# Kernel optimization log

Measured on AMD Instinct MI355X. Metric: run time of the kernel, lower is better.

Reference implementation:

```python
import jax, jax.numpy as jnp
import numpy as np

B, L, H, NH = 4, 1024, 768, 12
HS = H // NH          # 64
DPB_DIM = H // 4      # 192
TEMPERATURE = 1.0


def setup_inputs() -> dict:
    key = jax.random.key(0)
    ks = jax.random.split(key, 10)
    def xavier(k, shape):
        fan_in, fan_out = shape[0], shape[-1]
        std = (2.0 / (fan_in + fan_out)) ** 0.5
        return jax.random.normal(k, shape, dtype=jnp.float32) * std
    return {
        "x": jax.random.normal(ks[0], (B, L, H), dtype=jnp.float32),
        "adj": jax.random.normal(ks[1], (B, 1, L, L), dtype=jnp.float32),
        "mask": jnp.ones((B, L), dtype=bool),
        "weights": xavier(ks[2], (H, 3 * H)),
        "in_bias": jnp.zeros((1, 1, 3 * H), dtype=jnp.float32),
        "out_bias": jnp.zeros((1, 1, H), dtype=jnp.float32),
        "dpb_w0": xavier(ks[3], (1, DPB_DIM)),
        "dpb_b0": jnp.zeros((DPB_DIM,), dtype=jnp.float32),
        "dpb_w1": xavier(ks[4], (DPB_DIM, DPB_DIM)),
        "dpb_b1": jnp.zeros((DPB_DIM,), dtype=jnp.float32),
        "dpb_w2": xavier(ks[5], (DPB_DIM, NH)),
        "dpb_b2": jnp.zeros((NH,), dtype=jnp.float32),
    }


def _dyn_pos_bias(n, w0, b0, w1, b1, w2, b2):
    # relative positions -(n-1)..(n-1) -> per-head bias [NH, n, n]
    pos = jnp.arange(-n + 1, n, dtype=jnp.float32)[:, None]      # [2n-1, 1]
    hdn = jax.nn.silu(pos @ w0 + b0)
    hdn = jax.nn.silu(hdn @ w1 + b1)
    table = hdn @ w2 + b2                                        # [2n-1, NH]
    idx = jnp.arange(n)[:, None] - jnp.arange(n)[None, :] + (n - 1)  # [n, n]
    return jnp.transpose(table[idx], (2, 0, 1))                  # [NH, n, n]


def reference(x, adj, mask, weights, in_bias, out_bias,
              dpb_w0, dpb_b0, dpb_w1, dpb_b1, dpb_w2, dpb_b2):
    b, l, h = x.shape
    qkv = x @ weights + in_bias                                  # [b, l, 3h]
    # view(b,l,NH,-1).permute(0,2,1,3).chunk(3, dim=3): split 3*HS per head
    qkv = jnp.transpose(qkv.reshape(b, l, NH, 3 * HS), (0, 2, 1, 3))  # [b,NH,l,3HS]
    Q, K, V = qkv[..., :HS], qkv[..., HS:2 * HS], qkv[..., 2 * HS:]
    norm = HS ** 0.5
    attention = jnp.einsum('bhid,bhjd->bhij', Q, K) / TEMPERATURE / norm
    raw_attention = attention                                    # returned pre-bias
    attn_bias = _dyn_pos_bias(l, dpb_w0, dpb_b0, dpb_w1, dpb_b1, dpb_w2, dpb_b2)
    attention = attention + attn_bias[None] + adj
    mask_value = -jnp.finfo(attention.dtype).max
    attention = jnp.where(mask[:, None, None, :], attention, mask_value)
    attention = jax.nn.softmax(attention, axis=-1)
    out = attention @ V                                          # [b,NH,l,HS]
    out = jnp.transpose(out, (0, 2, 1, 3)).reshape(b, l, h)
    out = out + out_bias
    return (out, raw_attention)
```

## Files before the change

### kernel.cpp

```cpp
#include <hip/hip_runtime.h>
#include <stdint.h>
#include <stddef.h>


#define BB 4
#define LL 1024
#define NHH 12
#define HSS 64
#define HH 768
#define OUT_ELEMS (BB * LL * HH)
#define QKV_ELEMS (BB * NHH * LL * HSS)
#define X_ELEMS (BB * LL * HH)
#define W_ELEMS (HH * 3 * HH)

typedef __attribute__((ext_vector_type(8))) short short8;
typedef __attribute__((ext_vector_type(4))) float f32x4;

__device__ __forceinline__ ushort f2bf(float f) {
    union { float f; unsigned int i; } v; v.f = f;
    unsigned int r = v.i + 0x7FFFu + ((v.i >> 16) & 1u);
    return (ushort)(r >> 16);
}

__global__ void sentinel_kernel(float* out) {
    if (threadIdx.x == 0) out[0] = 12345.0f;
}

__global__ __launch_bounds__(256)
void cvt_bf16(const float* __restrict__ src, ushort* __restrict__ dst, int n) {
    int i = (blockIdx.x * 256 + threadIdx.x) * 8;
    if (i >= n) return;
    float4 a = *(const float4*)(src + i);
    float4 b = *(const float4*)(src + i + 4);
    short8 o;
    o[0] = (short)f2bf(a.x); o[1] = (short)f2bf(a.y);
    o[2] = (short)f2bf(a.z); o[3] = (short)f2bf(a.w);
    o[4] = (short)f2bf(b.x); o[5] = (short)f2bf(b.y);
    o[6] = (short)f2bf(b.z); o[7] = (short)f2bf(b.w);
    *(short8*)(dst + i) = o;
}

__global__ void dpb_kernel(const float* __restrict__ w0, const float* __restrict__ b0,
                           const float* __restrict__ w1, const float* __restrict__ b1,
                           const float* __restrict__ w2, const float* __restrict__ b2,
                           float* __restrict__ table) {
    __shared__ float h0s[192];
    __shared__ float h1s[192];
    int r = blockIdx.x, j = threadIdx.x;
    double pos = (double)(r - 1023);
    double a = pos * (double)w0[j] + (double)b0[j];
    h0s[j] = (float)(a / (1.0 + exp(-a)));
    __syncthreads();
    double acc = (double)b1[j];
    for (int k = 0; k < 192; ++k) acc += (double)h0s[k] * (double)w1[k * 192 + j];
    h1s[j] = (float)(acc / (1.0 + exp(-acc)));
    __syncthreads();
    if (j < 12) {
        double t = (double)b2[j];
        for (int k = 0; k < 192; ++k) t += (double)h1s[k] * (double)w2[k * 12 + j];
        table[r * 12 + j] = (float)t;
    }
}

__global__ __launch_bounds__(256)
void qkv_mfma(const ushort* __restrict__ x, const ushort* __restrict__ w,
              const float* __restrict__ bias,
              ushort* __restrict__ Qb, ushort* __restrict__ Kb, ushort* __restrict__ Vb) {
    __shared__ ushort As[64][32];
    __shared__ ushort Bts[64][56];

    int m0 = blockIdx.y * 64, n0 = blockIdx.x * 64;
    int tid = threadIdx.x, lane = tid & 63, wid = tid >> 6;
    int wr = wid >> 1, wc = wid & 1;
    int g = lane >> 4, qi = lane & 15;
    f32x4 acc[2][2] = {};

    int arow = tid >> 2, acol = (tid & 3) * 8;
    int bn = tid & 63, bkb = (tid >> 6) * 8;

    for (int k0 = 0; k0 < 768; k0 += 32) {
        short8 av = *(const short8*)(x + (size_t)(m0 + arow) * 768 + k0 + acol);
        ushort bt[8];
        #pragma unroll
        for (int i = 0; i < 8; ++i)
            bt[i] = w[(size_t)(k0 + bkb + i) * 2304 + n0 + bn];
        *(short8*)&As[arow][acol] = av;
        short8 bv;
        #pragma unroll
        for (int i = 0; i < 8; ++i) bv[i] = (short)bt[i];
        *(short8*)&Bts[bn][bkb] = bv;
        __syncthreads();

        short8 af0 = *(const short8*)&As[wr * 32 + qi][g * 8];
        short8 af1 = *(const short8*)&As[wr * 32 + 16 + qi][g * 8];
        short8 bf0 = *(const short8*)&Bts[wc * 32 + qi][g * 8];
        short8 bf1 = *(const short8*)&Bts[wc * 32 + 16 + qi][g * 8];
        acc[0][0] = __builtin_amdgcn_mfma_f32_16x16x32_bf16(af0, bf0, acc[0][0], 0, 0, 0);
        acc[0][1] = __builtin_amdgcn_mfma_f32_16x16x32_bf16(af0, bf1, acc[0][1], 0, 0, 0);
        acc[1][0] = __builtin_amdgcn_mfma_f32_16x16x32_bf16(af1, bf0, acc[1][0], 0, 0, 0);
        acc[1][1] = __builtin_amdgcn_mfma_f32_16x16x32_bf16(af1, bf1, acc[1][1], 0, 0, 0);
        __syncthreads();
    }

    #pragma unroll
    for (int ti = 0; ti < 2; ++ti)
    #pragma unroll
    for (int tj = 0; tj < 2; ++tj)
    #pragma unroll
    for (int r = 0; r < 4; ++r) {
        int row = m0 + wr * 32 + ti * 16 + g * 4 + r;
        int col = n0 + wc * 32 + tj * 16 + qi;
        float val = acc[ti][tj][r] + bias[col];
        int h = col / 192, rem = col % 192;
        int which = rem >> 6, d = rem & 63;
        int bb = row >> 10, ll = row & 1023;
        ushort* dst = which == 0 ? Qb : (which == 1 ? Kb : Vb);
        dst[(((size_t)(bb * 12 + h) * 1024 + ll) << 6) + d] = f2bf(val);
    }
}

__global__ __launch_bounds__(256)
void attn_mfma(const ushort* __restrict__ Qb, const ushort* __restrict__ Kb,
               const ushort* __restrict__ Vb, const float* __restrict__ adj,
               const float* __restrict__ table, const float* __restrict__ out_bias,
               float* __restrict__ out, float* __restrict__ raw) {
    __shared__ ushort Ks[32][72];
    __shared__ ushort Vt[64][72];
    __shared__ ushort Ps[4][16][40];

    int blk = blockIdx.x;
    int lb = (blk & 7) * 96 + (blk >> 3);
    int qb = lb & 15;
    int bh = lb >> 4;
    int h = bh % 12;
    int b = bh / 12;
    int q0 = qb * 64;
    int tid = threadIdx.x, lane = tid & 63, wid = tid >> 6;
    int g = lane >> 4, qi = lane & 15;
    int qg = q0 + wid * 16 + qi;

    short8 qfrag[2];
    qfrag[0] = *(const short8*)(Qb + ((size_t)(bh * 1024 + qg) << 6) + g * 8);
    qfrag[1] = *(const short8*)(Qb + ((size_t)(bh * 1024 + qg) << 6) + 32 + g * 8);

    float m = -INFINITY, ssum = 0.f;
    f32x4 oacc[4] = {};

    int srow = tid >> 3, scol = (tid & 7) * 8;
    int vd = tid & 63, vjb = (tid >> 6) * 8;

    for (int j0 = 0; j0 < 1024; j0 += 32) {
        short8 kv = *(const short8*)(Kb + ((size_t)(bh * 1024 + j0 + srow) << 6) + scol);
        ushort vt8[8];
        #pragma unroll
        for (int i = 0; i < 8; ++i)
            vt8[i] = Vb[((size_t)(bh * 1024 + j0 + vjb + i) << 6) + vd];
        *(short8*)&Ks[srow][scol] = kv;
        short8 vv;
        #pragma unroll
        for (int i = 0; i < 8; ++i) vv[i] = (short)vt8[i];
        *(short8*)&Vt[vd][vjb] = vv;
        __syncthreads();

        f32x4 sacc[2];
        #pragma unroll
        for (int jt = 0; jt < 2; ++jt) {
            short8 kf0 = *(const short8*)&Ks[jt * 16 + qi][g * 8];
            short8 kf1 = *(const short8*)&Ks[jt * 16 + qi][32 + g * 8];
            f32x4 z = {0.f, 0.f, 0.f, 0.f};
            z = __builtin_amdgcn_mfma_f32_16x16x32_bf16(kf0, qfrag[0], z, 0, 0, 0);
            z = __builtin_amdgcn_mfma_f32_16x16x32_bf16(kf1, qfrag[1], z, 0, 0, 0);
            sacc[jt] = z;
        }

        float lg[8];
        #pragma unroll
        for (int jt = 0; jt < 2; ++jt) {
            int jbase = j0 + jt * 16 + g * 4;
            f32x4 sv = sacc[jt] * 0.125f;
            *(f32x4*)(raw + ((size_t)(bh * 1024 + qg) << 10) + jbase) = sv;
            float4 av = *(const float4*)(adj + ((size_t)(b * 1024 + qg) << 10) + jbase);
            int tidx = (1023 + qg - jbase) * 12 + h;
            lg[jt * 4 + 0] = sv[0] + table[tidx] + av.x;
            lg[jt * 4 + 1] = sv[1] + table[tidx - 12] + av.y;
            lg[jt * 4 + 2] = sv[2] + table[tidx - 24] + av.z;
            lg[jt * 4 + 3] = sv[3] + table[tidx - 36] + av.w;
        }

        float cmax = lg[0];
        #pragma unroll
        for (int i = 1; i < 8; ++i) cmax = fmaxf(cmax, lg[i]);
        cmax = fmaxf(cmax, __shfl_xor(cmax, 16));
        cmax = fmaxf(cmax, __shfl_xor(cmax, 32));
        float newm = fmaxf(m, cmax);
        float corr = __expf(m - newm);
        float p[8], csum = 0.f;
        #pragma unroll
        for (int i = 0; i < 8; ++i) { p[i] = __expf(lg[i] - newm); csum += p[i]; }
        csum += __shfl_xor(csum, 16);
        csum += __shfl_xor(csum, 32);
        ssum = ssum * corr + csum;
        m = newm;
        #pragma unroll
        for (int dt = 0; dt < 4; ++dt) oacc[dt] *= corr;

        #pragma unroll
        for (int jt = 0; jt < 2; ++jt) {
            ushort4 pw;
            #pragma unroll
            for (int r = 0; r < 4; ++r) ((ushort*)&pw)[r] = f2bf(p[jt * 4 + r]);
            *(ushort4*)&Ps[wid][qi][jt * 16 + g * 4] = pw;
        }
        short8 pf = *(const short8*)&Ps[wid][qi][g * 8];
        #pragma unroll
        for (int dt = 0; dt < 4; ++dt) {
            short8 vf = *(const short8*)&Vt[dt * 16 + qi][g * 8];
            oacc[dt] = __builtin_amdgcn_mfma_f32_16x16x32_bf16(vf, pf, oacc[dt], 0, 0, 0);
        }
        __syncthreads();
    }

    float inv = 1.f / ssum;
    #pragma unroll
    for (int dt = 0; dt < 4; ++dt) {
        float4 ob = *(const float4*)(out_bias + h * 64 + dt * 16 + g * 4);
        f32x4 ov;
        ov[0] = oacc[dt][0] * inv + ob.x;
        ov[1] = oacc[dt][1] * inv + ob.y;
        ov[2] = oacc[dt][2] * inv + ob.z;
        ov[3] = oacc[dt][3] * inv + ob.w;
        *(f32x4*)(out + (size_t)(b * 1024 + qg) * 768 + h * 64 + dt * 16 + g * 4) = ov;
    }
}

extern "C" void kernel_launch(void* const* d_in, const int* in_sizes, int n_in,
                              void* d_out, int out_size, void* d_ws, size_t ws_size,
                              hipStream_t stream) {
    const float* x        = (const float*)d_in[0];
    const float* adj      = (const float*)d_in[1];
    const float* weights  = (const float*)d_in[3];
    const float* in_bias  = (const float*)d_in[4];
    const float* out_bias = (const float*)d_in[5];
    const float* dpb_w0   = (const float*)d_in[6];
    const float* dpb_b0   = (const float*)d_in[7];
    const float* dpb_w1   = (const float*)d_in[8];
    const float* dpb_b1   = (const float*)d_in[9];
    const float* dpb_w2   = (const float*)d_in[10];
    const float* dpb_b2   = (const float*)d_in[11];

    float* out = (float*)d_out;
    float* raw = out + OUT_ELEMS;

    float*  table = (float*)d_ws;
    ushort* xb    = (ushort*)((char*)d_ws + 98304);
    ushort* wb    = xb + X_ELEMS;
    ushort* Qb    = wb + W_ELEMS;
    ushort* Kb    = Qb + QKV_ELEMS;
    ushort* Vb    = Kb + QKV_ELEMS;
    size_t need = 98304 + (size_t)X_ELEMS * 2 + (size_t)W_ELEMS * 2
                + 3 * (size_t)QKV_ELEMS * 2;
    if (ws_size < need) {
        sentinel_kernel<<<1, 64, 0, stream>>>(out);
        return;
    }

    cvt_bf16<<<X_ELEMS / (256 * 8), 256, 0, stream>>>(x, xb, X_ELEMS);
    cvt_bf16<<<W_ELEMS / (256 * 8), 256, 0, stream>>>(weights, wb, W_ELEMS);
    dpb_kernel<<<2047, 192, 0, stream>>>(dpb_w0, dpb_b0, dpb_w1, dpb_b1, dpb_w2, dpb_b2, table);
    qkv_mfma<<<dim3(2304 / 64, 4096 / 64), 256, 0, stream>>>(xb, wb, in_bias, Qb, Kb, Vb);
    attn_mfma<<<768, 256, 0, stream>>>(Qb, Kb, Vb, adj, table, out_bias, out, raw);
}
```

Baseline: 173.3 us.

## Split attention over key halves, fuse bf16 conversion into QKV GEMM

Drops the separate fp32-to-bf16 conversion kernels for x and weights and converts inside the QKV GEMM load path instead. The attention kernel now splits the key range into two halves (split-K flash attention), doubling the block count to 1536. It processes 64 keys per iteration with register prefetch of the next K/V tile and caches the positional-bias slice in shared memory. A new combine kernel merges the two partial outputs using the saved max and sum, at the cost of an extra bf16 partial-output round trip and one more launch.

Measured after the change: 147.7 us. 1.17x faster.

```diff
diff --git a/kernel.cpp b/kernel.cpp
--- a/kernel.cpp
+++ b/kernel.cpp
@@ -10,12 +10,13 @@
 #define HH 768
 #define OUT_ELEMS (BB * LL * HH)
 #define QKV_ELEMS (BB * NHH * LL * HSS)
-#define X_ELEMS (BB * LL * HH)
-#define W_ELEMS (HH * 3 * HH)
 
 typedef __attribute__((ext_vector_type(8))) short short8;
 typedef __attribute__((ext_vector_type(4))) float f32x4;
 
+__device__ __forceinline__ float bf2f(ushort u) {
+    union { unsigned int i; float f; } v; v.i = ((unsigned int)u) << 16; return v.f;
+}
 __device__ __forceinline__ ushort f2bf(float f) {
     union { float f; unsigned int i; } v; v.f = f;
     unsigned int r = v.i + 0x7FFFu + ((v.i >> 16) & 1u);
@@ -24,20 +25,6 @@
 
 __global__ void sentinel_kernel(float* out) {
     if (threadIdx.x == 0) out[0] = 12345.0f;
-}
-
-__global__ __launch_bounds__(256)
-void cvt_bf16(const float* __restrict__ src, ushort* __restrict__ dst, int n) {
-    int i = (blockIdx.x * 256 + threadIdx.x) * 8;
-    if (i >= n) return;
-    float4 a = *(const float4*)(src + i);
-    float4 b = *(const float4*)(src + i + 4);
-    short8 o;
-    o[0] = (short)f2bf(a.x); o[1] = (short)f2bf(a.y);
-    o[2] = (short)f2bf(a.z); o[3] = (short)f2bf(a.w);
-    o[4] = (short)f2bf(b.x); o[5] = (short)f2bf(b.y);
-    o[6] = (short)f2bf(b.z); o[7] = (short)f2bf(b.w);
-    *(short8*)(dst + i) = o;
 }
 
 __global__ void dpb_kernel(const float* __restrict__ w0, const float* __restrict__ b0,
@@ -63,7 +50,7 @@
 }
 
 __global__ __launch_bounds__(256)
-void qkv_mfma(const ushort* __restrict__ x, const ushort* __restrict__ w,
+void qkv_mfma(const float* __restrict__ x, const float* __restrict__ w,
               const float* __restrict__ bias,
               ushort* __restrict__ Qb, ushort* __restrict__ Kb, ushort* __restrict__ Vb) {
     __shared__ ushort As[64][32];
@@ -79,15 +66,20 @@
     int bn = tid & 63, bkb = (tid >> 6) * 8;
 
     for (int k0 = 0; k0 < 768; k0 += 32) {
-        short8 av = *(const short8*)(x + (size_t)(m0 + arow) * 768 + k0 + acol);
-        ushort bt[8];
+        float4 a0 = *(const float4*)(x + (size_t)(m0 + arow) * 768 + k0 + acol);
+        float4 a1 = *(const float4*)(x + (size_t)(m0 + arow) * 768 + k0 + acol + 4);
+        float bt[8];
         #pragma unroll
         for (int i = 0; i < 8; ++i)
             bt[i] = w[(size_t)(k0 + bkb + i) * 2304 + n0 + bn];
+        short8 av, bv;
+        av[0] = (short)f2bf(a0.x); av[1] = (short)f2bf(a0.y);
+        av[2] = (short)f2bf(a0.z); av[3] = (short)f2bf(a0.w);
+        av[4] = (short)f2bf(a1.x); av[5] = (short)f2bf(a1.y);
+        av[6] = (short)f2bf(a1.z); av[7] = (short)f2bf(a1.w);
+        #pragma unroll
+        for (int i = 0; i < 8; ++i) bv[i] = (short)f2bf(bt[i]);
         *(short8*)&As[arow][acol] = av;
-        short8 bv;
-        #pragma unroll
-        for (int i = 0; i < 8; ++i) bv[i] = (short)bt[i];
         *(short8*)&Bts[bn][bkb] = bv;
         __syncthreads();
 
@@ -122,22 +114,31 @@
 __global__ __launch_bounds__(256)
 void attn_mfma(const ushort* __restrict__ Qb, const ushort* __restrict__ Kb,
                const ushort* __restrict__ Vb, const float* __restrict__ adj,
-               const float* __restrict__ table, const float* __restrict__ out_bias,
-               float* __restrict__ out, float* __restrict__ raw) {
-    __shared__ ushort Ks[32][72];
+               const float* __restrict__ table,
+               ushort* __restrict__ Opart, float* __restrict__ MZ,
+               float* __restrict__ raw) {
+    __shared__ ushort Ks[64][72];
     __shared__ ushort Vt[64][72];
-    __shared__ ushort Ps[4][16][40];
+    __shared__ ushort Ps[4][16][72];
+    __shared__ float  tbl[576];
 
     int blk = blockIdx.x;
-    int lb = (blk & 7) * 96 + (blk >> 3);
-    int qb = lb & 15;
-    int bh = lb >> 4;
+    int lb = (blk & 7) * 192 + (blk >> 3);
+    int bh = lb >> 5;
+    int rest = lb & 31;
+    int half = rest >> 4;
+    int qb = rest & 15;
     int h = bh % 12;
     int b = bh / 12;
     int q0 = qb * 64;
+    int j_start = half * 512;
     int tid = threadIdx.x, lane = tid & 63, wid = tid >> 6;
     int g = lane >> 4, qi = lane & 15;
     int qg = q0 + wid * 16 + qi;
+    int qrel = wid * 16 + qi;
+
+    int tbase = q0 - j_start + 512;
+    for (int i = tid; i < 575; i += 256) tbl[i] = table[(tbase + i) * 12 + h];
 
     short8 qfrag[2];
     qfrag[0] = *(const short8*)(Qb + ((size_t)(bh * 1024 + qg) << 6) + g * 8);
@@ -146,25 +147,46 @@
     float m = -INFINITY, ssum = 0.f;
     f32x4 oacc[4] = {};
 
-    int srow = tid >> 3, scol = (tid & 7) * 8;
-    int vd = tid & 63, vjb = (tid >> 6) * 8;
-
-    for (int j0 = 0; j0 < 1024; j0 += 32) {
-        short8 kv = *(const short8*)(Kb + ((size_t)(bh * 1024 + j0 + srow) << 6) + scol);
-        ushort vt8[8];
-        #pragma unroll
-        for (int i = 0; i < 8; ++i)
-            vt8[i] = Vb[((size_t)(bh * 1024 + j0 + vjb + i) << 6) + vd];
-        *(short8*)&Ks[srow][scol] = kv;
-        short8 vv;
-        #pragma unroll
-        for (int i = 0; i < 8; ++i) vv[i] = (short)vt8[i];
-        *(short8*)&Vt[vd][vjb] = vv;
+    int krow = tid >> 2, kcol = (tid & 3) * 16;
+    int vd = tid & 63, vjb = (tid >> 6) * 16;
+
+    short8 kr0, kr1, vr0, vr1;
+    {
+        const ushort* kp = Kb + ((size_t)(bh * 1024 + j_start + krow) << 6) + kcol;
+        kr0 = *(const short8*)kp;
+        kr1 = *(const short8*)(kp + 8);
+        ushort tmp[16];
+        #pragma unroll
+        for (int i = 0; i < 16; ++i)
+            tmp[i] = Vb[((size_t)(bh * 1024 + j_start + vjb + i) << 6) + vd];
+        #pragma unroll
+        for (int i = 0; i < 8; ++i) { vr0[i] = (short)tmp[i]; vr1[i] = (short)tmp[i + 8]; }
+    }
+
+    for (int it = 0; it < 8; ++it) {
+        int j0 = j_start + it * 64;
+        *(short8*)&Ks[krow][kcol] = kr0;
+        *(short8*)&Ks[krow][kcol + 8] = kr1;
+        *(short8*)&Vt[vd][vjb] = vr0;
+        *(short8*)&Vt[vd][vjb + 8] = vr1;
         __syncthreads();
 
-        f32x4 sacc[2];
-        #pragma unroll
-        for (int jt = 0; jt < 2; ++jt) {
+        if (it < 7) {
+            int jn = j0 + 64;
+            const ushort* kp = Kb + ((size_t)(bh * 1024 + jn + krow) << 6) + kcol;
+            kr0 = *(const short8*)kp;
+            kr1 = *(const short8*)(kp + 8);
+            ushort tmp[16];
+            #pragma unroll
+            for (int i = 0; i < 16; ++i)
+                tmp[i] = Vb[((size_t)(bh * 1024 + jn + vjb + i) << 6) + vd];
+            #pragma unroll
+            for (int i = 0; i < 8; ++i) { vr0[i] = (short)tmp[i]; vr1[i] = (short)tmp[i + 8]; }
+        }
+
+        f32x4 sacc[4];
+        #pragma unroll
+        for (int jt = 0; jt < 4; ++jt) {
             short8 kf0 = *(const short8*)&Ks[jt * 16 + qi][g * 8];
             short8 kf1 = *(const short8*)&Ks[jt * 16 + qi][32 + g * 8];
             f32x4 z = {0.f, 0.f, 0.f, 0.f};
@@ -173,30 +195,30 @@
             sacc[jt] = z;
         }
 
-        float lg[8];
-        #pragma unroll
-        for (int jt = 0; jt < 2; ++jt) {
+        float lg[16];
+        #pragma unroll
+        for (int jt = 0; jt < 4; ++jt) {
             int jbase = j0 + jt * 16 + g * 4;
             f32x4 sv = sacc[jt] * 0.125f;
             *(f32x4*)(raw + ((size_t)(bh * 1024 + qg) << 10) + jbase) = sv;
             float4 av = *(const float4*)(adj + ((size_t)(b * 1024 + qg) << 10) + jbase);
-            int tidx = (1023 + qg - jbase) * 12 + h;
-            lg[jt * 4 + 0] = sv[0] + table[tidx] + av.x;
-            lg[jt * 4 + 1] = sv[1] + table[tidx - 12] + av.y;
-            lg[jt * 4 + 2] = sv[2] + table[tidx - 24] + av.z;
-            lg[jt * 4 + 3] = sv[3] + table[tidx - 36] + av.w;
+            int ib = qrel + j_start + 511 - jbase;
+            lg[jt * 4 + 0] = sv[0] + tbl[ib] + av.x;
+            lg[jt * 4 + 1] = sv[1] + tbl[ib - 1] + av.y;
+            lg[jt * 4 + 2] = sv[2] + tbl[ib - 2] + av.z;
+            lg[jt * 4 + 3] = sv[3] + tbl[ib - 3] + av.w;
         }
 
         float cmax = lg[0];
         #pragma unroll
-        for (int i = 1; i < 8; ++i) cmax = fmaxf(cmax, lg[i]);
+        for (int i = 1; i < 16; ++i) cmax = fmaxf(cmax, lg[i]);
         cmax = fmaxf(cmax, __shfl_xor(cmax, 16));
         cmax = fmaxf(cmax, __shfl_xor(cmax, 32));
         float newm = fmaxf(m, cmax);
         float corr = __expf(m - newm);
-        float p[8], csum = 0.f;
-        #pragma unroll
-        for (int i = 0; i < 8; ++i) { p[i] = __expf(lg[i] - newm); csum += p[i]; }
+        float p[16], csum = 0.f;
+        #pragma unroll
+        for (int i = 0; i < 16; ++i) { p[i] = __expf(lg[i] - newm); csum += p[i]; }
         csum += __shfl_xor(csum, 16);
         csum += __shfl_xor(csum, 32);
         ssum = ssum * corr + csum;
@@ -205,32 +227,67 @@
         for (int dt = 0; dt < 4; ++dt) oacc[dt] *= corr;
 
         #pragma unroll
-        for (int jt = 0; jt < 2; ++jt) {
+        for (int jt = 0; jt < 4; ++jt) {
             ushort4 pw;
             #pragma unroll
             for (int r = 0; r < 4; ++r) ((ushort*)&pw)[r] = f2bf(p[jt * 4 + r]);
             *(ushort4*)&Ps[wid][qi][jt * 16 + g * 4] = pw;
         }
-        short8 pf = *(const short8*)&Ps[wid][qi][g * 8];
+        short8 pf0 = *(const short8*)&Ps[wid][qi][g * 8];
+        short8 pf1 = *(const short8*)&Ps[wid][qi][32 + g * 8];
         #pragma unroll
         for (int dt = 0; dt < 4; ++dt) {
-            short8 vf = *(const short8*)&Vt[dt * 16 + qi][g * 8];
-            oacc[dt] = __builtin_amdgcn_mfma_f32_16x16x32_bf16(vf, pf, oacc[dt], 0, 0, 0);
+            short8 vf0 = *(const short8*)&Vt[dt * 16 + qi][g * 8];
+            short8 vf1 = *(const short8*)&Vt[dt * 16 + qi][32 + g * 8];
+            oacc[dt] = __builtin_amdgcn_mfma_f32_16x16x32_bf16(vf0, pf0, oacc[dt], 0, 0, 0);
+            oacc[dt] = __builtin_amdgcn_mfma_f32_16x16x32_bf16(vf1, pf1, oacc[dt], 0, 0, 0);
         }
         __syncthreads();
     }
 
-    float inv = 1.f / ssum;
+    int pb = (bh * 16 + qb) * 2 + half;
     #pragma unroll
     for (int dt = 0; dt < 4; ++dt) {
-        float4 ob = *(const float4*)(out_bias + h * 64 + dt * 16 + g * 4);
-        f32x4 ov;
-        ov[0] = oacc[dt][0] * inv + ob.x;
-        ov[1] = oacc[dt][1] * inv + ob.y;
-        ov[2] = oacc[dt][2] * inv + ob.z;
-        ov[3] = oacc[dt][3] * inv + ob.w;
-        *(f32x4*)(out + (size_t)(b * 1024 + qg) * 768 + h * 64 + dt * 16 + g * 4) = ov;
-    }
+        ushort4 ow;
+        #pragma unroll
+        for (int r = 0; r < 4; ++r) ((ushort*)&ow)[r] = f2bf(oacc[dt][r]);
+        *(ushort4*)(Opart + (size_t)pb * 4096 + qrel * 64 + dt * 16 + g * 4) = ow;
+    }
+    if (g == 0) {
+        MZ[pb * 128 + qrel * 2] = m;
+        MZ[pb * 128 + qrel * 2 + 1] = ssum;
+    }
+}
+
+__global__ __launch_bounds__(256)
+void combine_kernel(const ushort* __restrict__ Opart, const float* __restrict__ MZ,
+                    const float* __restrict__ out_bias, float* __restrict__ out) {
+    int cb = blockIdx.x;
+    int bh = cb >> 4, qb = cb & 15;
+    int h = bh % 12, b = bh / 12;
+    int t = threadIdx.x;
+    int q = t >> 2, dg = (t & 3) * 16;
+    int p0 = cb * 2, p1 = p0 + 1;
+    float m0 = MZ[p0 * 128 + q * 2], Z0 = MZ[p0 * 128 + q * 2 + 1];
+    float m1 = MZ[p1 * 128 + q * 2], Z1 = MZ[p1 * 128 + q * 2 + 1];
+    float mm = fmaxf(m0, m1);
+    float a0 = __expf(m0 - mm), a1 = __expf(m1 - mm);
+    float inv = 1.f / (a0 * Z0 + a1 * Z1);
+    const ushort* r0 = Opart + (size_t)p0 * 4096 + q * 64 + dg;
+    const ushort* r1 = Opart + (size_t)p1 * 4096 + q * 64 + dg;
+    short8 x0a = *(const short8*)r0, x0b = *(const short8*)(r0 + 8);
+    short8 x1a = *(const short8*)r1, x1b = *(const short8*)(r1 + 8);
+    float* op = out + (size_t)(b * 1024 + qb * 64 + q) * 768 + h * 64 + dg;
+    const float* ob = out_bias + h * 64 + dg;
+    float res[16];
+    #pragma unroll
+    for (int i = 0; i < 8; ++i) {
+        res[i]     = (a0 * bf2f((ushort)x0a[i]) + a1 * bf2f((ushort)x1a[i])) * inv + ob[i];
+        res[i + 8] = (a0 * bf2f((ushort)x0b[i]) + a1 * bf2f((ushort)x1b[i])) * inv + ob[i + 8];
+    }
+    #pragma unroll
+    for (int i = 0; i < 4; ++i)
+        *(float4*)(op + i * 4) = *(float4*)(res + i * 4);
 }
 
 extern "C" void kernel_launch(void* const* d_in, const int* in_sizes, int n_in,
@@ -252,21 +309,20 @@
     float* raw = out + OUT_ELEMS;
 
     float*  table = (float*)d_ws;
-    ushort* xb    = (ushort*)((char*)d_ws + 98304);
-    ushort* wb    = xb + X_ELEMS;
-    ushort* Qb    = wb + W_ELEMS;
+    ushort* Qb    = (ushort*)((char*)d_ws + 98304);
     ushort* Kb    = Qb + QKV_ELEMS;
     ushort* Vb    = Kb + QKV_ELEMS;
-    size_t need = 98304 + (size_t)X_ELEMS * 2 + (size_t)W_ELEMS * 2
-                + 3 * (size_t)QKV_ELEMS * 2;
+    ushort* Opart = Vb + QKV_ELEMS;
+    float*  MZ    = (float*)(Opart + (size_t)1536 * 4096);
+    size_t need = 98304 + 3 * (size_t)QKV_ELEMS * 2
+                + (size_t)1536 * 4096 * 2 + (size_t)1536 * 128 * 4;
     if (ws_size < need) {
         sentinel_kernel<<<1, 64, 0, stream>>>(out);
         return;
     }
 
-    cvt_bf16<<<X_ELEMS / (256 * 8), 256, 0, stream>>>(x, xb, X_ELEMS);
-    cvt_bf16<<<W_ELEMS / (256 * 8), 256, 0, stream>>>(weights, wb, W_ELEMS);
     dpb_kernel<<<2047, 192, 0, stream>>>(dpb_w0, dpb_b0, dpb_w1, dpb_b1, dpb_w2, dpb_b2, table);
-    qkv_mfma<<<dim3(2304 / 64, 4096 / 64), 256, 0, stream>>>(xb, wb, in_bias, Qb, Kb, Vb);
-    attn_mfma<<<768, 256, 0, stream>>>(Qb, Kb, Vb, adj, table, out_bias, out, raw);
-}
+    qkv_mfma<<<dim3(2304 / 64, 4096 / 64), 256, 0, stream>>>(x, weights, in_bias, Qb, Kb, Vb);
+    attn_mfma<<<1536, 256, 0, stream>>>(Qb, Kb, Vb, adj, table, Opart, MZ, raw);
+    combine_kernel<<<768, 256, 0, stream>>>(Opart, MZ, out_bias, out);
+}
```
